# Kernel optimization log

Hardware: AMD Instinct MI355X
Metric: run time of the kernel (lower is better)

Reference implementation:

```python
import jax, jax.numpy as jnp
import numpy as np

B, C, H, W = 16, 512, 25, 25
HEADS = 8
HID = 2048
PATCH = 5  # hardcoded patch_size in FusionAttention
EPS_LN = 1e-5
EPS_BN = 1e-5


def _channel_layernorm(x, g, b):
    # torch: std = var(unbiased=False).sqrt(); (x-mean)/(std+eps)*g + b, over channel dim=1
    mean = jnp.mean(x, axis=1, keepdims=True)
    var = jnp.var(x, axis=1, keepdims=True)
    return (x - mean) / (jnp.sqrt(var) + EPS_LN) * g + b


def _dwconv3x3(x, w, b):
    # depthwise 3x3, padding 1; w: (C,1,3,3)
    y = jax.lax.conv_general_dilated(
        x, w, window_strides=(1, 1), padding=((1, 1), (1, 1)),
        feature_group_count=x.shape[1],
        dimension_numbers=('NCHW', 'OIHW', 'NCHW'))
    return y + b[None, :, None, None]


def setup_inputs() -> dict:
    key = jax.random.key(0)
    ks = jax.random.split(key, 20)
    s = 0.02
    d = {
        'x': jax.random.normal(ks[0], (B, C, H, W), jnp.float32),
        'ln1_g': jnp.ones((1, C, 1, 1), jnp.float32),
        'ln1_b': jnp.zeros((1, C, 1, 1), jnp.float32),
        'wq': jax.random.normal(ks[1], (C, 1, 3, 3), jnp.float32) * s,
        'bq': jnp.zeros((C,), jnp.float32),
        'wk': jax.random.normal(ks[2], (C, 1, 3, 3), jnp.float32) * s,
        'bk': jnp.zeros((C,), jnp.float32),
        'wv': jax.random.normal(ks[3], (C, 1, 3, 3), jnp.float32) * s,
        'bv': jnp.zeros((C,), jnp.float32),
        'swq': jax.random.normal(ks[4], (C, 1, 3, 3), jnp.float32) * s,
        'sbq': jnp.zeros((C,), jnp.float32),
        'swk': jax.random.normal(ks[5], (C, 1, 3, 3), jnp.float32) * s,
        'sbk': jnp.zeros((C,), jnp.float32),
        'swv': jax.random.normal(ks[6], (C, 1, 3, 3), jnp.float32) * s,
        'sbv': jnp.zeros((C,), jnp.float32),
        'proj_w': jax.random.normal(ks[7], (C, C, 1, 1), jnp.float32) * s,
        'bn_g': jnp.ones((C,), jnp.float32),
        'bn_b': jnp.zeros((C,), jnp.float32),
        'bn_mean': jnp.zeros((C,), jnp.float32),
        'bn_var': jnp.ones((C,), jnp.float32),
        'ln2_g': jnp.ones((1, C, 1, 1), jnp.float32),
        'ln2_b': jnp.zeros((1, C, 1, 1), jnp.float32),
        'w1': jax.random.normal(ks[8], (HID, C, 1, 1), jnp.float32) * s,
        'b1': jnp.zeros((HID,), jnp.float32),
        'w2': jax.random.normal(ks[9], (C, HID, 1, 1), jnp.float32) * s,
        'b2': jnp.zeros((C,), jnp.float32),
    }
    return d


def _fusion_attention(x, wq, bq, wk, bk, wv, bv, swq, sbq, swk, sbk, swv, sbv,
                      proj_w, bn_g, bn_b, bn_mean, bn_var):
    b, c, h, w = x.shape
    n = h * w
    hd = c // HEADS
    scale = hd ** -0.5

    def split_heads(t):  # (b,c,h,w) -> (b, heads, n, hd)
        return t.reshape(b, HEADS, hd, n).transpose(0, 1, 3, 2)

    q = split_heads(_dwconv3x3(x, wq, bq))
    k = split_heads(_dwconv3x3(x, wk, bk))
    v = split_heads(_dwconv3x3(x, wv, bv))

    dots = jnp.einsum('bhid,bhjd->bhij', q, k) * scale
    attn = jax.nn.softmax(dots, axis=-1)
    out = jnp.einsum('bhij,bhjd->bhid', attn, v)
    # rearrange 'b h (H W) d -> b (h d) H W' with H=PATCH
    out = out.transpose(0, 1, 3, 2).reshape(b, c, PATCH, n // PATCH)

    spe_q = _dwconv3x3(out, swq, sbq).reshape(b, c, n)          # b d (l w)
    spe_k = _dwconv3x3(out, swk, sbk).reshape(b, c, n).transpose(0, 2, 1)  # b (l w) d
    spe_v = _dwconv3x3(out, swv, sbv).reshape(b, c, n)

    attention = jax.nn.softmax(jnp.einsum('bcn,bnd->bcd', spe_q, spe_k) * scale, axis=-1)
    x_out = jnp.einsum('bcd,bdn->bcn', attention, spe_v).reshape(b, c, h, w)

    # 1x1 conv (no bias) + BatchNorm2d (eval mode)
    proj = jnp.einsum('oc,bchw->bohw', proj_w[:, :, 0, 0], x_out)
    proj = (proj - bn_mean[None, :, None, None]) / jnp.sqrt(bn_var + EPS_BN)[None, :, None, None]
    proj = proj * bn_g[None, :, None, None] + bn_b[None, :, None, None]
    return proj


def _feedforward(x, w1, b1, w2, b2):
    h1 = jnp.einsum('oc,bchw->bohw', w1[:, :, 0, 0], x) + b1[None, :, None, None]
    h1 = jax.nn.gelu(h1, approximate=False)
    return jnp.einsum('oc,bchw->bohw', w2[:, :, 0, 0], h1) + b2[None, :, None, None]


def reference(x, ln1_g, ln1_b, wq, bq, wk, bk, wv, bv, swq, sbq, swk, sbk,
              swv, sbv, proj_w, bn_g, bn_b, bn_mean, bn_var, ln2_g, ln2_b,
              w1, b1, w2, b2):
    y1 = x + _fusion_attention(_channel_layernorm(x, ln1_g, ln1_b),
                               wq, bq, wk, bk, wv, bv, swq, sbq, swk, sbk,
                               swv, sbv, proj_w, bn_g, bn_b, bn_mean, bn_var)
    y_out = y1 + _feedforward(_channel_layernorm(y1, ln2_g, ln2_b), w1, b1, w2, b2)
    return y_out
```

## Files before the change

### kernel.cpp

```cpp
#include <hip/hip_runtime.h>
#include <math.h>

constexpr int BATCH = 16;
constexpr int CH    = 512;
constexpr int NPIX  = 625;
constexpr int HEADS = 8;
constexpr int HDIM  = 64;
constexpr int HIDD  = 2048;

constexpr float EPS_LN = 1e-5f;
constexpr float EPS_BN = 1e-5f;
constexpr float SCALE  = 0.125f;

typedef __bf16 bf16x8 __attribute__((ext_vector_type(8)));
typedef float  f32x4  __attribute__((ext_vector_type(4)));

__global__ void ln_kernel(const float* __restrict__ x, const float* __restrict__ g,
                          const float* __restrict__ bt, float* __restrict__ y) {
  int i = blockIdx.x * blockDim.x + threadIdx.x;
  int b = blockIdx.y;
  if (i >= NPIX) return;
  const float* xb = x + ((size_t)b * CH) * NPIX + i;
  float s = 0.f, ss = 0.f;
  for (int c = 0; c < CH; ++c) {
    float v = xb[(size_t)c * NPIX];
    s += v; ss += v * v;
  }
  float mean = s * (1.0f / CH);
  float var  = ss * (1.0f / CH) - mean * mean;
  float inv  = 1.0f / (sqrtf(fmaxf(var, 0.0f)) + EPS_LN);
  float* yb = y + ((size_t)b * CH) * NPIX + i;
  for (int c = 0; c < CH; ++c) {
    float v = xb[(size_t)c * NPIX];
    yb[(size_t)c * NPIX] = (v - mean) * inv * g[c] + bt[c];
  }
}

__global__ void dwconv3_kernel(const float* __restrict__ src,
    const float* __restrict__ w0, const float* __restrict__ b0,
    const float* __restrict__ w1, const float* __restrict__ b1,
    const float* __restrict__ w2, const float* __restrict__ b2,
    float* __restrict__ d0, float* __restrict__ d1, float* __restrict__ d2,
    int Hc, int Wc) {
  size_t idx = (size_t)blockIdx.x * blockDim.x + threadIdx.x;
  size_t total = (size_t)BATCH * CH * Hc * Wc;
  if (idx >= total) return;
  int wp = (int)(idx % Wc);
  int hp = (int)((idx / Wc) % Hc);
  int c  = (int)((idx / ((size_t)Wc * Hc)) % CH);
  const float* f0 = w0 + c * 9;
  const float* f1 = w1 + c * 9;
  const float* f2 = w2 + c * 9;
  float a0 = 0.f, a1 = 0.f, a2 = 0.f;
  #pragma unroll
  for (int kh = -1; kh <= 1; ++kh) {
    int h2 = hp + kh; if (h2 < 0 || h2 >= Hc) continue;
    #pragma unroll
    for (int kw = -1; kw <= 1; ++kw) {
      int w2p = wp + kw; if (w2p < 0 || w2p >= Wc) continue;
      float v = src[idx + (size_t)kh * Wc + kw];
      int wi = (kh + 1) * 3 + (kw + 1);
      a0 += v * f0[wi]; a1 += v * f1[wi]; a2 += v * f2[wi];
    }
  }
  d0[idx] = a0 + b0[c];
  d1[idx] = a1 + b1[c];
  d2[idx] = a2 + b2[c];
}

__global__ void dwconv_spe_kernel(const float* __restrict__ src,
    const float* __restrict__ w0, const float* __restrict__ b0,
    const float* __restrict__ w1, const float* __restrict__ b1,
    const float* __restrict__ w2, const float* __restrict__ b2,
    __bf16* __restrict__ q16, __bf16* __restrict__ k16, float* __restrict__ v) {
  size_t idx = (size_t)blockIdx.x * blockDim.x + threadIdx.x;
  if (idx >= (size_t)BATCH * CH * 640) return;
  int n = (int)(idx % 640);
  int c = (int)((idx / 640) % CH);
  int b = (int)(idx / ((size_t)640 * CH));
  if (n >= NPIX) { q16[idx] = (__bf16)0.f; k16[idx] = (__bf16)0.f; return; }
  int hp = n / 125, wp = n % 125;
  size_t base = ((size_t)b * CH + c) * NPIX;
  const float* f0 = w0 + c * 9;
  const float* f1 = w1 + c * 9;
  const float* f2 = w2 + c * 9;
  float a0 = 0.f, a1 = 0.f, a2 = 0.f;
  #pragma unroll
  for (int kh = -1; kh <= 1; ++kh) {
    int h2 = hp + kh; if (h2 < 0 || h2 >= 5) continue;
    #pragma unroll
    for (int kw = -1; kw <= 1; ++kw) {
      int w2p = wp + kw; if (w2p < 0 || w2p >= 125) continue;
      float vv = src[base + h2 * 125 + w2p];
      int wi = (kh + 1) * 3 + (kw + 1);
      a0 += vv * f0[wi]; a1 += vv * f1[wi]; a2 += vv * f2[wi];
    }
  }
  q16[idx] = (__bf16)(a0 + b0[c]);
  k16[idx] = (__bf16)(a1 + b1[c]);
  v[base + n] = a2 + b2[c];
}

__global__ __launch_bounds__(256) void qk_to_bf16T(
    const float* __restrict__ q, const float* __restrict__ k,
    __bf16* __restrict__ qT, __bf16* __restrict__ kT) {
  __shared__ __bf16 tq[64][65];
  __shared__ __bf16 tk[64][65];
  int bh = blockIdx.y;
  int n0 = blockIdx.x * 64;
  int b = bh >> 3, h = bh & 7;
  const float* qb = q + (size_t)(b * CH + h * HDIM) * NPIX;
  const float* kb = k + (size_t)(b * CH + h * HDIM) * NPIX;
  #pragma unroll
  for (int it = 0; it < 16; ++it) {
    int idx = threadIdx.x + it * 256;
    int d = idx >> 6, n = idx & 63;
    int nn = n0 + n;
    float qv = (nn < NPIX) ? qb[(size_t)d * NPIX + nn] : 0.f;
    float kv = (nn < NPIX) ? kb[(size_t)d * NPIX + nn] : 0.f;
    tq[n][d] = (__bf16)qv;
    tk[n][d] = (__bf16)kv;
  }
  __syncthreads();
  size_t obase = (size_t)bh * NPIX;
  #pragma unroll
  for (int it = 0; it < 16; ++it) {
    int idx = threadIdx.x + it * 256;
    int n = idx >> 6, d = idx & 63;
    int nn = n0 + n;
    if (nn < NPIX) {
      qT[(obase + nn) * 64 + d] = tq[n][d];
      kT[(obase + nn) * 64 + d] = tk[n][d];
    }
  }
}

__global__ void v_to_bf16(const float* __restrict__ v, __bf16* __restrict__ v16) {
  int row = blockIdx.x;
  const float* src = v + (size_t)row * NPIX;
  __bf16* dst = v16 + (size_t)row * 640;
  for (int n = threadIdx.x; n < NPIX; n += 256) dst[n] = (__bf16)src[n];
}

__global__ __launch_bounds__(256) void head_attn_mfma(
    const __bf16* __restrict__ qT, const __bf16* __restrict__ kT,
    const __bf16* __restrict__ vB, float* __restrict__ out) {
  __shared__ __align__(16) unsigned char sm_p[4][2048];
  __shared__ float lds_o[4][64][17];
  int t = threadIdx.x;
  int w = t >> 6, lane = t & 63, g = lane >> 4, li = lane & 15;
  int h = blockIdx.y, b = blockIdx.z;
  int bh = b * HEADS + h;
  int i0w = blockIdx.x * 64 + w * 16;
  const __bf16* Qb = qT + (size_t)bh * NPIX * 64;
  const __bf16* Kb = kT + (size_t)bh * NPIX * 64;
  const __bf16* Vb = vB + (size_t)(b * CH + h * HDIM) * 640;

  bf16x8 aq0, aq1;
  {
    int qr = i0w + li; if (qr > NPIX - 1) qr = NPIX - 1;
    const __bf16* qp = Qb + (size_t)qr * 64 + 8 * g;
    aq0 = *(const bf16x8*)(qp);
    aq1 = *(const bf16x8*)(qp + 32);
  }

  f32x4 o[4];
  #pragma unroll
  for (int dg = 0; dg < 4; ++dg) o[dg] = (f32x4){0.f, 0.f, 0.f, 0.f};
  float m[4] = {-1e30f, -1e30f, -1e30f, -1e30f};
  float l[4] = {0.f, 0.f, 0.f, 0.f};

  for (int jt = 0; jt < 10; ++jt) {
    int j0 = jt * 64;
    f32x4 s[4];
    #pragma unroll
    for (int cg = 0; cg < 4; ++cg) {
      int kc = j0 + cg * 16 + li;
      int kcc = kc > NPIX - 1 ? NPIX - 1 : kc;
      const __bf16* kp = Kb + (size_t)kcc * 64 + 8 * g;
      bf16x8 bk0 = *(const bf16x8*)(kp);
      bf16x8 bk1 = *(const bf16x8*)(kp + 32);
      f32x4 acc = (f32x4){0.f, 0.f, 0.f, 0.f};
      acc = __builtin_amdgcn_mfma_f32_16x16x32_bf16(aq0, bk0, acc, 0, 0, 0);
      acc = __builtin_amdgcn_mfma_f32_16x16x32_bf16(aq1, bk1, acc, 0, 0, 0);
      acc = acc * SCALE;
      if (kc > NPIX - 1) {
        acc[0] = -1e30f; acc[1] = -1e30f; acc[2] = -1e30f; acc[3] = -1e30f;
      }
      s[cg] = acc;
    }
    #pragma unroll
    for (int rr = 0; rr < 4; ++rr) {
      float mv = fmaxf(fmaxf(s[0][rr], s[1][rr]), fmaxf(s[2][rr], s[3][rr]));
      mv = fmaxf(mv, __shfl_xor(mv, 1));
      mv = fmaxf(mv, __shfl_xor(mv, 2));
      mv = fmaxf(mv, __shfl_xor(mv, 4));
      mv = fmaxf(mv, __shfl_xor(mv, 8));
      float mn = fmaxf(m[rr], mv);
      float corr = __expf(m[rr] - mn);
      m[rr] = mn;
      float rs = 0.f;
      #pragma unroll
      for (int cg = 0; cg < 4; ++cg) {
        float p = __expf(s[cg][rr] - mn);
        s[cg][rr] = p;
        rs += p;
      }
      rs += __shfl_xor(rs, 1);
      rs += __shfl_xor(rs, 2);
      rs += __shfl_xor(rs, 4);
      rs += __shfl_xor(rs, 8);
      l[rr] = l[rr] * corr + rs;
      #pragma unroll
      for (int dg = 0; dg < 4; ++dg) o[dg][rr] *= corr;
    }
    #pragma unroll
    for (int cg = 0; cg < 4; ++cg) {
      #pragma unroll
      for (int rr = 0; rr < 4; ++rr) {
        int row = 4 * g + rr, col = cg * 16 + li;
        int off = (row * 128 + col * 2) ^ ((row & 7) << 4);
        *(__bf16*)(&sm_p[w][off]) = (__bf16)s[cg][rr];
      }
    }
    int off0 = li * 128 + ((16 * g) ^ ((li & 7) << 4));
    int off1 = li * 128 + ((16 * g + 64) ^ ((li & 7) << 4));
    bf16x8 pa0 = *(const bf16x8*)(&sm_p[w][off0]);
    bf16x8 pa1 = *(const bf16x8*)(&sm_p[w][off1]);
    const __bf16* vp = Vb + (size_t)li * 640 + j0 + 8 * g;
    #pragma unroll
    for (int dg = 0; dg < 4; ++dg) {
      const __bf16* vpp = vp + (size_t)dg * 16 * 640;
      bf16x8 bv0 = *(const bf16x8*)(vpp);
      bf16x8 bv1 = *(const bf16x8*)(vpp + 32);
      o[dg] = __builtin_amdgcn_mfma_f32_16x16x32_bf16(pa0, bv0, o[dg], 0, 0, 0);
      o[dg] = __builtin_amdgcn_mfma_f32_16x16x32_bf16(pa1, bv1, o[dg], 0, 0, 0);
    }
  }

  float invl[4];
  #pragma unroll
  for (int rr = 0; rr < 4; ++rr) invl[rr] = 1.0f / l[rr];
  #pragma unroll
  for (int dg = 0; dg < 4; ++dg) {
    #pragma unroll
    for (int rr = 0; rr < 4; ++rr)
      lds_o[w][dg * 16 + li][4 * g + rr] = o[dg][rr] * invl[rr];
  }
  size_t cbase = (size_t)(b * CH + h * HDIM);
  int n = i0w + li;
  #pragma unroll
  for (int dd = 0; dd < 16; ++dd) {
    int d = dd * 4 + g;
    if (n < NPIX) out[(cbase + d) * NPIX + n] = lds_o[w][d][li];
  }
}

__global__ __launch_bounds__(64) void chan_attn_mfma(
    const __bf16* __restrict__ sq, const __bf16* __restrict__ sk,
    __bf16* __restrict__ Am) {
  int lane = threadIdx.x & 63;
  int g = lane >> 4, li = lane & 15;
  int b = blockIdx.y;
  int cq0 = blockIdx.x * 16;
  const __bf16* qrow  = sq + ((size_t)b * CH + cq0 + li) * 640 + 8 * g;
  const __bf16* kbase = sk + ((size_t)b * CH + li) * 640 + 8 * g;
  f32x4 acc[32];
  #pragma unroll
  for (int i = 0; i < 32; ++i) acc[i] = (f32x4){0.f, 0.f, 0.f, 0.f};
  for (int ks = 0; ks < 20; ++ks) {
    bf16x8 af = *(const bf16x8*)(qrow + ks * 32);
    #pragma unroll
    for (int cf = 0; cf < 32; ++cf) {
      bf16x8 bfr = *(const bf16x8*)(kbase + (size_t)cf * 16 * 640 + ks * 32);
      acc[cf] = __builtin_amdgcn_mfma_f32_16x16x32_bf16(af, bfr, acc[cf], 0, 0, 0);
    }
  }
  #pragma unroll
  for (int i = 0; i < 32; ++i) acc[i] = acc[i] * SCALE;
  __bf16* Ab = Am + ((size_t)b * CH + cq0) * CH;
  #pragma unroll
  for (int r = 0; r < 4; ++r) {
    float mx = -1e30f;
    #pragma unroll
    for (int cf = 0; cf < 32; ++cf) mx = fmaxf(mx, acc[cf][r]);
    mx = fmaxf(mx, __shfl_xor(mx, 1));
    mx = fmaxf(mx, __shfl_xor(mx, 2));
    mx = fmaxf(mx, __shfl_xor(mx, 4));
    mx = fmaxf(mx, __shfl_xor(mx, 8));
    float sum = 0.f;
    #pragma unroll
    for (int cf = 0; cf < 32; ++cf) {
      float p = __expf(acc[cf][r] - mx);
      acc[cf][r] = p;
      sum += p;
    }
    sum += __shfl_xor(sum, 1);
    sum += __shfl_xor(sum, 2);
    sum += __shfl_xor(sum, 4);
    sum += __shfl_xor(sum, 8);
    float inv = 1.0f / sum;
    #pragma unroll
    for (int cf = 0; cf < 32; ++cf)
      Ab[(size_t)(4 * g + r) * CH + cf * 16 + li] = (__bf16)(acc[cf][r] * inv);
  }
}

template <int EPI>
__global__ __launch_bounds__(256) void gemm_nt(
    const __bf16* __restrict__ A, long long aBatch,
    const __bf16* __restrict__ B, long long bBatch,
    void* __restrict__ Cout, long long cBatch,
    int M, int N, int K,
    const float* __restrict__ p0, const float* __restrict__ p1,
    const float* __restrict__ res, long long resBatch) {
  __shared__ __align__(16) union {
    struct { unsigned char As[128 * 128]; unsigned char Bs[64 * 128]; } s;
    float Ce[4][64][17];
  } u;
  int t = threadIdx.x;
  int w = t >> 6, lane = t & 63, g = lane >> 4, li = lane & 15;
  int wm = w & 1, wn = w >> 1;
  int n0 = blockIdx.x * 64, m0 = blockIdx.y * 128, b = blockIdx.z;
  const __bf16* Ab = A + (size_t)b * aBatch;
  const __bf16* Bb = B + (size_t)b * bBatch;
  f32x4 acc[4][2];
  #pragma unroll
  for (int i = 0; i < 4; ++i)
    #pragma unroll
    for (int j = 0; j < 2; ++j) acc[i][j] = (f32x4){0.f, 0.f, 0.f, 0.f};

  for (int k0 = 0; k0 < K; k0 += 64) {
    bf16x8 ra[4], rb[2];
    #pragma unroll
    for (int i = 0; i < 4; ++i) {
      int e = t + i * 256;
      int row = e >> 3, cc = e & 7;
      int ar = m0 + row; ar = ar < M ? ar : M - 1;
      ra[i] = *(const bf16x8*)(Ab + (size_t)ar * K + k0 + cc * 8);
    }
    #pragma unroll
    for (int i = 0; i < 2; ++i) {
      int e = t + i * 256;
      int row = e >> 3, cc = e & 7;
      rb[i] = *(const bf16x8*)(Bb + (size_t)(n0 + row) * K + k0 + cc * 8);
    }
    __syncthreads();
    #pragma unroll
    for (int i = 0; i < 4; ++i) {
      int e = t + i * 256; int row = e >> 3, cc = e & 7;
      int off = (row * 128 + cc * 16) ^ ((row & 7) << 4);
      *(bf16x8*)(&u.s.As[off]) = ra[i];
    }
    #pragma unroll
    for (int i = 0; i < 2; ++i) {
      int e = t + i * 256; int row = e >> 3, cc = e & 7;
      int off = (row * 128 + cc * 16) ^ ((row & 7) << 4);
      *(bf16x8*)(&u.s.Bs[off]) = rb[i];
    }
    __syncthreads();
    #pragma unroll
    for (int ks = 0; ks < 2; ++ks) {
      bf16x8 af[4], bfr[2];
      #pragma unroll
      for (int mf = 0; mf < 4; ++mf) {
        int row = wm * 64 + mf * 16 + li;
        int off = (row * 128 + ks * 64 + g * 16) ^ ((row & 7) << 4);
        af[mf] = *(const bf16x8*)(&u.s.As[off]);
      }
      #pragma unroll
      for (int nf = 0; nf < 2; ++nf) {
        int row = wn * 32 + nf * 16 + li;
        int off = (row * 128 + ks * 64 + g * 16) ^ ((row & 7) << 4);
        bfr[nf] = *(const bf16x8*)(&u.s.Bs[off]);
      }
      #pragma unroll
      for (int mf = 0; mf < 4; ++mf)
        #pragma unroll
        for (int nf = 0; nf < 2; ++nf)
          acc[mf][nf] = __builtin_amdgcn_mfma_f32_16x16x32_bf16(
              af[mf], bfr[nf], acc[mf][nf], 0, 0, 0);
    }
    __syncthreads();
  }

  #pragma unroll
  for (int p = 0; p < 2; ++p) {
    __syncthreads();
    #pragma unroll
    for (int mf = 0; mf < 4; ++mf) {
      #pragma unroll
      for (int r = 0; r < 4; ++r)
        u.Ce[w][mf * 16 + 4 * g + r][li] = acc[mf][p][r];
    }
    __syncthreads();
    int m = m0 + wm * 64 + lane;
    int colb = n0 + wn * 32 + p * 16;
    if (m < M) {
      float vv[16];
      #pragma unroll
      for (int c = 0; c < 16; ++c) vv[c] = u.Ce[w][lane][c];
      if (EPI == 0) {
        __bf16* Cb = (__bf16*)Cout + (size_t)b * cBatch + (size_t)m * N + colb;
        bf16x8 o0, o1;
        #pragma unroll
        for (int j = 0; j < 8; ++j) { o0[j] = (__bf16)vv[j]; o1[j] = (__bf16)vv[8 + j]; }
        *(bf16x8*)(Cb) = o0;
        *(bf16x8*)(Cb + 8) = o1;
      } else if (EPI == 1) {
        float* Cf = (float*)Cout + (size_t)b * cBatch + (size_t)m * N + colb;
        const float* rp = res + (size_t)b * resBatch + (size_t)m * N + colb;
        #pragma unroll
        for (int c = 0; c < 16; ++c)
          vv[c] = vv[c] * p0[colb + c] + p1[colb + c] + rp[c];
        #pragma unroll
        for (int c4 = 0; c4 < 4; ++c4)
          *(f32x4*)(Cf + c4 * 4) = (f32x4){vv[c4*4], vv[c4*4+1], vv[c4*4+2], vv[c4*4+3]};
      } else if (EPI == 2) {
        __bf16* Cb = (__bf16*)Cout + (size_t)b * cBatch + (size_t)m * N + colb;
        #pragma unroll
        for (int c = 0; c < 16; ++c) {
          float xg = vv[c] + p0[colb + c];
          vv[c] = 0.5f * xg * (1.0f + erff(xg * 0.70710678118654752f));
        }
        bf16x8 o0, o1;
        #pragma unroll
        for (int j = 0; j < 8; ++j) { o0[j] = (__bf16)vv[j]; o1[j] = (__bf16)vv[8 + j]; }
        *(bf16x8*)(Cb) = o0;
        *(bf16x8*)(Cb + 8) = o1;
      } else {
        float* Cf = (float*)Cout + (size_t)b * cBatch + (size_t)m * N + colb;
        const float* rp = res + (size_t)b * resBatch + (size_t)m * N + colb;
        #pragma unroll
        for (int c = 0; c < 16; ++c)
          vv[c] = vv[c] + p0[colb + c] + rp[c];
        #pragma unroll
        for (int c4 = 0; c4 < 4; ++c4)
          *(f32x4*)(Cf + c4 * 4) = (f32x4){vv[c4*4], vv[c4*4+1], vv[c4*4+2], vv[c4*4+3]};
      }
    }
  }
}

template <typename TO>
__global__ __launch_bounds__(256) void transpose_bat(
    const float* __restrict__ in, TO* __restrict__ out, int R, int Cc) {
  __shared__ float tile[64][65];
  int b = blockIdx.z;
  int c0 = blockIdx.x * 64, r0 = blockIdx.y * 64;
  const float* ib = in + (size_t)b * R * Cc;
  TO* ob = out + (size_t)b * R * Cc;
  for (int e = threadIdx.x; e < 4096; e += 256) {
    int rr = e >> 6, cc = e & 63;
    int r = r0 + rr, c = c0 + cc;
    tile[rr][cc] = (r < R && c < Cc) ? ib[(size_t)r * Cc + c] : 0.f;
  }
  __syncthreads();
  for (int e = threadIdx.x; e < 4096; e += 256) {
    int cc = e >> 6, rr = e & 63;
    int r = r0 + rr, c = c0 + cc;
    if (r < R && c < Cc) ob[(size_t)c * R + r] = (TO)tile[rr][cc];
  }
}

__global__ __launch_bounds__(256) void ln2_row_kernel(
    const float* __restrict__ y, const float* __restrict__ g,
    const float* __restrict__ bt, __bf16* __restrict__ o) {
  int row = blockIdx.x * 4 + (threadIdx.x >> 6);
  int lane = threadIdx.x & 63;
  const float* yr = y + (size_t)row * CH + lane * 8;
  f32x4 v0 = *(const f32x4*)(yr);
  f32x4 v1 = *(const f32x4*)(yr + 4);
  float s = v0[0]+v0[1]+v0[2]+v0[3]+v1[0]+v1[1]+v1[2]+v1[3];
  float ss = v0[0]*v0[0]+v0[1]*v0[1]+v0[2]*v0[2]+v0[3]*v0[3]
           + v1[0]*v1[0]+v1[1]*v1[1]+v1[2]*v1[2]+v1[3]*v1[3];
  #pragma unroll
  for (int off = 32; off > 0; off >>= 1) {
    s  += __shfl_xor(s, off);
    ss += __shfl_xor(ss, off);
  }
  float mean = s * (1.0f / CH);
  float var  = ss * (1.0f / CH) - mean * mean;
  float inv  = 1.0f / (sqrtf(fmaxf(var, 0.0f)) + EPS_LN);
  f32x4 g0 = *(const f32x4*)(g + lane * 8);
  f32x4 g1 = *(const f32x4*)(g + lane * 8 + 4);
  f32x4 b0 = *(const f32x4*)(bt + lane * 8);
  f32x4 b1 = *(const f32x4*)(bt + lane * 8 + 4);
  bf16x8 ov;
  #pragma unroll
  for (int j = 0; j < 4; ++j) ov[j]     = (__bf16)((v0[j] - mean) * inv * g0[j] + b0[j]);
  #pragma unroll
  for (int j = 0; j < 4; ++j) ov[4 + j] = (__bf16)((v1[j] - mean) * inv * g1[j] + b1[j]);
  *(bf16x8*)(o + (size_t)row * CH + lane * 8) = ov;
}

__global__ void cast_bf16_kernel(const float* __restrict__ s, __bf16* __restrict__ d, int n) {
  int i = blockIdx.x * 256 + threadIdx.x;
  if (i < n) d[i] = (__bf16)s[i];
}

__global__ void bn_prep(const float* __restrict__ g, const float* __restrict__ bt,
                        const float* __restrict__ mean, const float* __restrict__ var,
                        float* __restrict__ scale, float* __restrict__ shift) {
  int c = blockIdx.x * blockDim.x + threadIdx.x;
  if (c >= CH) return;
  float s = g[c] * rsqrtf(var[c] + EPS_BN);
  scale[c] = s;
  shift[c] = bt[c] - mean[c] * s;
}

extern "C" void kernel_launch(void* const* d_in, const int* in_sizes, int n_in,
                              void* d_out, int out_size, void* d_ws, size_t ws_size,
                              hipStream_t stream) {
  const float* x      = (const float*)d_in[0];
  const float* ln1_g  = (const float*)d_in[1];
  const float* ln1_b  = (const float*)d_in[2];
  const float* wq     = (const float*)d_in[3];
  const float* bq     = (const float*)d_in[4];
  const float* wk     = (const float*)d_in[5];
  const float* bk     = (const float*)d_in[6];
  const float* wv     = (const float*)d_in[7];
  const float* bv     = (const float*)d_in[8];
  const float* swq    = (const float*)d_in[9];
  const float* sbq    = (const float*)d_in[10];
  const float* swk    = (const float*)d_in[11];
  const float* sbk    = (const float*)d_in[12];
  const float* swv    = (const float*)d_in[13];
  const float* sbv    = (const float*)d_in[14];
  const float* proj_w = (const float*)d_in[15];
  const float* bn_g   = (const float*)d_in[16];
  const float* bn_b   = (const float*)d_in[17];
  const float* bn_m   = (const float*)d_in[18];
  const float* bn_v   = (const float*)d_in[19];
  const float* ln2_g  = (const float*)d_in[20];
  const float* ln2_b  = (const float*)d_in[21];
  const float* w1     = (const float*)d_in[22];
  const float* b1     = (const float*)d_in[23];
  const float* w2     = (const float*)d_in[24];
  const float* b2     = (const float*)d_in[25];

  char* W = (char*)d_ws;
  const size_t SZB = 20480000;
  char* S0 = W;
  char* S1 = W + SZB;
  char* S2 = W + 2 * SZB;
  char* S3 = W + 3 * SZB;
  char* S4 = W + 4 * SZB;

  float*  xln   = (float*)S0;
  float*  qb    = (float*)S1;
  float*  kb    = (float*)S2;
  float*  vb    = (float*)S3;
  __bf16* qT    = (__bf16*)S0;
  __bf16* kTp   = qT + (size_t)BATCH * HEADS * NPIX * 64;
  __bf16* v16   = (__bf16*)d_out;
  float*  ab    = (float*)S4;
  __bf16* sq16  = (__bf16*)S1;
  __bf16* sk16  = (__bf16*)S2;
  float*  sv    = (float*)S3;
  __bf16* svT   = (__bf16*)S4;
  __bf16* Amat  = (__bf16*)S0;
  __bf16* pw16  = (__bf16*)(S0 + 10485760);
  __bf16* w116  = (__bf16*)(S0 + 10485760 + 524288);
  __bf16* w216  = (__bf16*)(S0 + 10485760 + 524288 + 2097152);
  float*  bnsc  = (float*)(S0 + 10485760 + 524288 + 2097152 + 2097152);
  float*  bnsh  = bnsc + CH;
  __bf16* xoutT = (__bf16*)S1;
  float*  x_nc  = (float*)S4;
  float*  y1_nc = (float*)S3;
  __bf16* y1ln  = (__bf16*)S0;
  __bf16* h1T   = (__bf16*)S1;
  float*  tmp_nc = (float*)S4;

  const size_t SZ = (size_t)BATCH * CH * NPIX;

  ln_kernel<<<dim3(3, BATCH), 256, 0, stream>>>(x, ln1_g, ln1_b, xln);
  dwconv3_kernel<<<(int)((SZ + 255) / 256), 256, 0, stream>>>(
      xln, wq, bq, wk, bk, wv, bv, qb, kb, vb, 25, 25);
  qk_to_bf16T<<<dim3(10, BATCH * HEADS), 256, 0, stream>>>(qb, kb, qT, kTp);
  v_to_bf16<<<dim3(BATCH * CH), 256, 0, stream>>>(vb, v16);
  head_attn_mfma<<<dim3(10, HEADS, BATCH), 256, 0, stream>>>(qT, kTp, v16, ab);
  dwconv_spe_kernel<<<(int)(((size_t)BATCH * CH * 640 + 255) / 256), 256, 0, stream>>>(
      ab, swq, sbq, swk, sbk, swv, sbv, sq16, sk16, sv);
  transpose_bat<__bf16><<<dim3(10, 8, BATCH), 256, 0, stream>>>(sv, svT, CH, NPIX);
  cast_bf16_kernel<<<1024, 256, 0, stream>>>(proj_w, pw16, CH * CH);
  cast_bf16_kernel<<<4096, 256, 0, stream>>>(w1, w116, HIDD * CH);
  cast_bf16_kernel<<<4096, 256, 0, stream>>>(w2, w216, CH * HIDD);
  bn_prep<<<2, 256, 0, stream>>>(bn_g, bn_b, bn_m, bn_v, bnsc, bnsh);
  chan_attn_mfma<<<dim3(32, BATCH), 64, 0, stream>>>(sq16, sk16, Amat);
  gemm_nt<0><<<dim3(8, 5, BATCH), 256, 0, stream>>>(
      svT, (long long)NPIX * CH, Amat, (long long)CH * CH,
      xoutT, (long long)NPIX * CH, NPIX, CH, CH,
      nullptr, nullptr, nullptr, 0);
  transpose_bat<float><<<dim3(10, 8, BATCH), 256, 0, stream>>>(x, x_nc, CH, NPIX);
  gemm_nt<1><<<dim3(8, 79, 1), 256, 0, stream>>>(
      xoutT, 0LL, pw16, 0LL, y1_nc, 0LL, BATCH * NPIX, CH, CH,
      bnsc, bnsh, x_nc, 0LL);
  ln2_row_kernel<<<BATCH * NPIX / 4, 256, 0, stream>>>(y1_nc, ln2_g, ln2_b, y1ln);
  gemm_nt<2><<<dim3(32, 79, 1), 256, 0, stream>>>(
      y1ln, 0LL, w116, 0LL, h1T, 0LL, BATCH * NPIX, HIDD, CH,
      b1, nullptr, nullptr, 0LL);
  gemm_nt<3><<<dim3(8, 79, 1), 256, 0, stream>>>(
      h1T, 0LL, w216, 0LL, tmp_nc, 0LL, BATCH * NPIX, CH, HIDD,
      b2, nullptr, y1_nc, 0LL);
  transpose_bat<float><<<dim3(8, 10, BATCH), 256, 0, stream>>>(
      tmp_nc, (float*)d_out, NPIX, CH);
}
```

Measured before the change: 646.8 us.

## Split LN1 channel reduction across warps and use single-pass register softmax attention

The first layernorm kernel now splits the channel reduction across four waves per block and combines partial sums in shared memory, launching 160 blocks instead of 48 for better GPU occupancy. The head attention kernel is rewritten as one 64-thread wave per 16 query rows. It holds all 640 key scores in registers and does an exact two-pass softmax instead of online rescaling, then stages the whole probability row in LDS for the PV MFMAs. This removes the per-tile rescale work and spreads the grid wider, at the cost of high register pressure from 40 f32x4 accumulators, which may spill or limit occupancy.

New measurement: 600.7 us. 1.08x faster.

```diff
diff --git a/kernel.cpp b/kernel.cpp
--- a/kernel.cpp
+++ b/kernel.cpp
@@ -15,22 +15,40 @@
 typedef __bf16 bf16x8 __attribute__((ext_vector_type(8)));
 typedef float  f32x4  __attribute__((ext_vector_type(4)));
 
-__global__ void ln_kernel(const float* __restrict__ x, const float* __restrict__ g,
-                          const float* __restrict__ bt, float* __restrict__ y) {
-  int i = blockIdx.x * blockDim.x + threadIdx.x;
-  int b = blockIdx.y;
-  if (i >= NPIX) return;
-  const float* xb = x + ((size_t)b * CH) * NPIX + i;
+static __device__ inline unsigned pack_bf16(float lo, float hi) {
+  union { __bf16 h; unsigned short u; } a, b;
+  a.h = (__bf16)lo; b.h = (__bf16)hi;
+  return ((unsigned)b.u << 16) | (unsigned)a.u;
+}
+
+__global__ __launch_bounds__(256) void ln_kernel2(
+    const float* __restrict__ x, const float* __restrict__ g,
+    const float* __restrict__ bt, float* __restrict__ y) {
+  __shared__ float ps[4][64];
+  __shared__ float pss[4][64];
+  int lane = threadIdx.x & 63;
+  int w    = threadIdx.x >> 6;
+  int b    = blockIdx.y;
+  int i    = blockIdx.x * 64 + lane;
+  int ic   = i < NPIX ? i : NPIX - 1;
+  const float* xb = x + (size_t)b * CH * NPIX + ic;
   float s = 0.f, ss = 0.f;
-  for (int c = 0; c < CH; ++c) {
+  #pragma unroll 4
+  for (int c = w * 128; c < w * 128 + 128; ++c) {
     float v = xb[(size_t)c * NPIX];
     s += v; ss += v * v;
   }
-  float mean = s * (1.0f / CH);
-  float var  = ss * (1.0f / CH) - mean * mean;
+  ps[w][lane] = s; pss[w][lane] = ss;
+  __syncthreads();
+  float st  = ps[0][lane] + ps[1][lane] + ps[2][lane] + ps[3][lane];
+  float sst = pss[0][lane] + pss[1][lane] + pss[2][lane] + pss[3][lane];
+  float mean = st * (1.0f / CH);
+  float var  = sst * (1.0f / CH) - mean * mean;
   float inv  = 1.0f / (sqrtf(fmaxf(var, 0.0f)) + EPS_LN);
-  float* yb = y + ((size_t)b * CH) * NPIX + i;
-  for (int c = 0; c < CH; ++c) {
+  if (i >= NPIX) return;
+  float* yb = y + (size_t)b * CH * NPIX + i;
+  #pragma unroll 4
+  for (int c = w * 128; c < w * 128 + 128; ++c) {
     float v = xb[(size_t)c * NPIX];
     yb[(size_t)c * NPIX] = (v - mean) * inv * g[c] + bt[c];
   }
@@ -142,117 +160,121 @@
   for (int n = threadIdx.x; n < NPIX; n += 256) dst[n] = (__bf16)src[n];
 }
 
-__global__ __launch_bounds__(256) void head_attn_mfma(
+__global__ __launch_bounds__(64) void head_attn_mfma2(
     const __bf16* __restrict__ qT, const __bf16* __restrict__ kT,
     const __bf16* __restrict__ vB, float* __restrict__ out) {
-  __shared__ __align__(16) unsigned char sm_p[4][2048];
-  __shared__ float lds_o[4][64][17];
-  int t = threadIdx.x;
-  int w = t >> 6, lane = t & 63, g = lane >> 4, li = lane & 15;
+  __shared__ __align__(16) union SmT {
+    unsigned char p[16 * 1280];
+    float ostage[64][17];
+  } sm;
+  int lane = threadIdx.x & 63;
+  int g = lane >> 4, li = lane & 15;
   int h = blockIdx.y, b = blockIdx.z;
   int bh = b * HEADS + h;
-  int i0w = blockIdx.x * 64 + w * 16;
+  int i0 = blockIdx.x * 16;
   const __bf16* Qb = qT + (size_t)bh * NPIX * 64;
   const __bf16* Kb = kT + (size_t)bh * NPIX * 64;
   const __bf16* Vb = vB + (size_t)(b * CH + h * HDIM) * 640;
 
   bf16x8 aq0, aq1;
   {
-    int qr = i0w + li; if (qr > NPIX - 1) qr = NPIX - 1;
+    int qr = i0 + li; if (qr > NPIX - 1) qr = NPIX - 1;
     const __bf16* qp = Qb + (size_t)qr * 64 + 8 * g;
     aq0 = *(const bf16x8*)(qp);
     aq1 = *(const bf16x8*)(qp + 32);
   }
 
+  f32x4 s[40];
+  #pragma unroll
+  for (int cf = 0; cf < 40; ++cf) {
+    int kc = cf * 16 + li;
+    int kcl = kc > NPIX - 1 ? NPIX - 1 : kc;
+    const __bf16* kp = Kb + (size_t)kcl * 64 + 8 * g;
+    bf16x8 bk0 = *(const bf16x8*)(kp);
+    bf16x8 bk1 = *(const bf16x8*)(kp + 32);
+    f32x4 acc = (f32x4){0.f, 0.f, 0.f, 0.f};
+    acc = __builtin_amdgcn_mfma_f32_16x16x32_bf16(aq0, bk0, acc, 0, 0, 0);
+    acc = __builtin_amdgcn_mfma_f32_16x16x32_bf16(aq1, bk1, acc, 0, 0, 0);
+    s[cf] = acc * SCALE;
+  }
+  if (li > 0) {
+    s[39][0] = -1e30f; s[39][1] = -1e30f; s[39][2] = -1e30f; s[39][3] = -1e30f;
+  }
+
+  #pragma unroll
+  for (int r = 0; r < 4; ++r) {
+    float mx = -1e30f;
+    #pragma unroll
+    for (int cf = 0; cf < 40; ++cf) mx = fmaxf(mx, s[cf][r]);
+    mx = fmaxf(mx, __shfl_xor(mx, 1));
+    mx = fmaxf(mx, __shfl_xor(mx, 2));
+    mx = fmaxf(mx, __shfl_xor(mx, 4));
+    mx = fmaxf(mx, __shfl_xor(mx, 8));
+    float sum = 0.f;
+    #pragma unroll
+    for (int cf = 0; cf < 40; ++cf) {
+      float p = __expf(s[cf][r] - mx);
+      s[cf][r] = p;
+      sum += p;
+    }
+    sum += __shfl_xor(sum, 1);
+    sum += __shfl_xor(sum, 2);
+    sum += __shfl_xor(sum, 4);
+    sum += __shfl_xor(sum, 8);
+    float inv = 1.0f / sum;
+    #pragma unroll
+    for (int cf = 0; cf < 40; ++cf) s[cf][r] *= inv;
+  }
+
+  #pragma unroll
+  for (int cfp = 0; cfp < 20; ++cfp) {
+    int cf0 = 2 * cfp, cf1 = cf0 + 1;
+    #pragma unroll
+    for (int r = 0; r < 4; ++r) {
+      float v0 = s[cf0][r], v1 = s[cf1][r];
+      float t0 = __shfl_xor(v0, 1);
+      float t1 = __shfl_xor(v1, 1);
+      bool even = (li & 1) == 0;
+      float lo = even ? v0 : t1;
+      float hi = even ? t0 : v1;
+      int col_w = even ? (cf0 * 16 + li) : (cf1 * 16 + li - 1);
+      int row = 4 * g + r;
+      int off = (row * 1280 + col_w * 2) ^ ((row & 7) << 4);
+      *(unsigned*)(&sm.p[off]) = pack_bf16(lo, hi);
+    }
+  }
+
   f32x4 o[4];
   #pragma unroll
   for (int dg = 0; dg < 4; ++dg) o[dg] = (f32x4){0.f, 0.f, 0.f, 0.f};
-  float m[4] = {-1e30f, -1e30f, -1e30f, -1e30f};
-  float l[4] = {0.f, 0.f, 0.f, 0.f};
-
-  for (int jt = 0; jt < 10; ++jt) {
-    int j0 = jt * 64;
-    f32x4 s[4];
-    #pragma unroll
-    for (int cg = 0; cg < 4; ++cg) {
-      int kc = j0 + cg * 16 + li;
-      int kcc = kc > NPIX - 1 ? NPIX - 1 : kc;
-      const __bf16* kp = Kb + (size_t)kcc * 64 + 8 * g;
-      bf16x8 bk0 = *(const bf16x8*)(kp);
-      bf16x8 bk1 = *(const bf16x8*)(kp + 32);
-      f32x4 acc = (f32x4){0.f, 0.f, 0.f, 0.f};
-      acc = __builtin_amdgcn_mfma_f32_16x16x32_bf16(aq0, bk0, acc, 0, 0, 0);
-      acc = __builtin_amdgcn_mfma_f32_16x16x32_bf16(aq1, bk1, acc, 0, 0, 0);
-      acc = acc * SCALE;
-      if (kc > NPIX - 1) {
-        acc[0] = -1e30f; acc[1] = -1e30f; acc[2] = -1e30f; acc[3] = -1e30f;
-      }
-      s[cg] = acc;
-    }
-    #pragma unroll
-    for (int rr = 0; rr < 4; ++rr) {
-      float mv = fmaxf(fmaxf(s[0][rr], s[1][rr]), fmaxf(s[2][rr], s[3][rr]));
-      mv = fmaxf(mv, __shfl_xor(mv, 1));
-      mv = fmaxf(mv, __shfl_xor(mv, 2));
-      mv = fmaxf(mv, __shfl_xor(mv, 4));
-      mv = fmaxf(mv, __shfl_xor(mv, 8));
-      float mn = fmaxf(m[rr], mv);
-      float corr = __expf(m[rr] - mn);
-      m[rr] = mn;
-      float rs = 0.f;
-      #pragma unroll
-      for (int cg = 0; cg < 4; ++cg) {
-        float p = __expf(s[cg][rr] - mn);
-        s[cg][rr] = p;
-        rs += p;
-      }
-      rs += __shfl_xor(rs, 1);
-      rs += __shfl_xor(rs, 2);
-      rs += __shfl_xor(rs, 4);
-      rs += __shfl_xor(rs, 8);
-      l[rr] = l[rr] * corr + rs;
-      #pragma unroll
-      for (int dg = 0; dg < 4; ++dg) o[dg][rr] *= corr;
-    }
-    #pragma unroll
-    for (int cg = 0; cg < 4; ++cg) {
-      #pragma unroll
-      for (int rr = 0; rr < 4; ++rr) {
-        int row = 4 * g + rr, col = cg * 16 + li;
-        int off = (row * 128 + col * 2) ^ ((row & 7) << 4);
-        *(__bf16*)(&sm_p[w][off]) = (__bf16)s[cg][rr];
-      }
-    }
-    int off0 = li * 128 + ((16 * g) ^ ((li & 7) << 4));
-    int off1 = li * 128 + ((16 * g + 64) ^ ((li & 7) << 4));
-    bf16x8 pa0 = *(const bf16x8*)(&sm_p[w][off0]);
-    bf16x8 pa1 = *(const bf16x8*)(&sm_p[w][off1]);
-    const __bf16* vp = Vb + (size_t)li * 640 + j0 + 8 * g;
+  #pragma unroll
+  for (int ks = 0; ks < 20; ++ks) {
+    int offr = (li * 1280 + ks * 64 + 16 * g) ^ ((li & 7) << 4);
+    bf16x8 pa = *(const bf16x8*)(&sm.p[offr]);
+    const __bf16* vp = Vb + (size_t)li * 640 + ks * 32 + 8 * g;
     #pragma unroll
     for (int dg = 0; dg < 4; ++dg) {
-      const __bf16* vpp = vp + (size_t)dg * 16 * 640;
-      bf16x8 bv0 = *(const bf16x8*)(vpp);
-      bf16x8 bv1 = *(const bf16x8*)(vpp + 32);
-      o[dg] = __builtin_amdgcn_mfma_f32_16x16x32_bf16(pa0, bv0, o[dg], 0, 0, 0);
-      o[dg] = __builtin_amdgcn_mfma_f32_16x16x32_bf16(pa1, bv1, o[dg], 0, 0, 0);
-    }
-  }
-
-  float invl[4];
-  #pragma unroll
-  for (int rr = 0; rr < 4; ++rr) invl[rr] = 1.0f / l[rr];
+      bf16x8 bv = *(const bf16x8*)(vp + (size_t)dg * 16 * 640);
+      o[dg] = __builtin_amdgcn_mfma_f32_16x16x32_bf16(pa, bv, o[dg], 0, 0, 0);
+    }
+  }
+
+  __syncthreads();
   #pragma unroll
   for (int dg = 0; dg < 4; ++dg) {
     #pragma unroll
-    for (int rr = 0; rr < 4; ++rr)
-      lds_o[w][dg * 16 + li][4 * g + rr] = o[dg][rr] * invl[rr];
-  }
+    for (int r = 0; r < 4; ++r)
+      sm.ostage[dg * 16 + li][4 * g + r] = o[dg][r];
+  }
+  __syncthreads();
   size_t cbase = (size_t)(b * CH + h * HDIM);
-  int n = i0w + li;
-  #pragma unroll
-  for (int dd = 0; dd < 16; ++dd) {
-    int d = dd * 4 + g;
-    if (n < NPIX) out[(cbase + d) * NPIX + n] = lds_o[w][d][li];
+  int n = i0 + li;
+  if (n < NPIX) {
+    #pragma unroll
+    for (int dd = 0; dd < 16; ++dd) {
+      int d = dd * 4 + g;
+      out[(cbase + d) * NPIX + n] = sm.ostage[d][li];
+    }
   }
 }
 
@@ -574,12 +596,12 @@
 
   const size_t SZ = (size_t)BATCH * CH * NPIX;
 
-  ln_kernel<<<dim3(3, BATCH), 256, 0, stream>>>(x, ln1_g, ln1_b, xln);
+  ln_kernel2<<<dim3(10, BATCH), 256, 0, stream>>>(x, ln1_g, ln1_b, xln);
   dwconv3_kernel<<<(int)((SZ + 255) / 256), 256, 0, stream>>>(
       xln, wq, bq, wk, bk, wv, bv, qb, kb, vb, 25, 25);
   qk_to_bf16T<<<dim3(10, BATCH * HEADS), 256, 0, stream>>>(qb, kb, qT, kTp);
   v_to_bf16<<<dim3(BATCH * CH), 256, 0, stream>>>(vb, v16);
-  head_attn_mfma<<<dim3(10, HEADS, BATCH), 256, 0, stream>>>(qT, kTp, v16, ab);
+  head_attn_mfma2<<<dim3(40, HEADS, BATCH), 64, 0, stream>>>(qT, kTp, v16, ab);
   dwconv_spe_kernel<<<(int)(((size_t)BATCH * CH * 640 + 255) / 256), 256, 0, stream>>>(
       ab, swq, sbq, swk, sbk, swv, sbv, sq16, sk16, sv);
   transpose_bat<__bf16><<<dim3(10, 8, BATCH), 256, 0, stream>>>(sv, svT, CH, NPIX);
```
